# Optimization experiments

Measured on AMD Instinct MI355X. Metric: run time of the kernel, lower is better.

## Reference

```python
import jax, jax.numpy as jnp
import numpy as np

B, N, D, H = 8, 2048, 1024, 1024

def setup_inputs() -> dict:
    key = jax.random.key(0)
    ks = jax.random.split(key, 7)
    s = 1.0 / np.sqrt(D)
    return {
        "x": jax.random.normal(ks[0], (B, N, D), dtype=jnp.float32),
        "Wq": jax.random.uniform(ks[1], (D, H), jnp.float32, -s, s),
        "bq": jax.random.uniform(ks[2], (H,), jnp.float32, -s, s),
        "Wk": jax.random.uniform(ks[3], (D, H), jnp.float32, -s, s),
        "bk": jax.random.uniform(ks[4], (H,), jnp.float32, -s, s),
        "Wv": jax.random.uniform(ks[5], (D, H), jnp.float32, -s, s),
        "bv": jax.random.uniform(ks[6], (H,), jnp.float32, -s, s),
    }

def reference(x, Wq, bq, Wk, bk, Wv, bv):
    # q, k, v: [B, N, H]
    q = jnp.einsum('bnd,dh->bnh', x, Wq) + bq
    k = jnp.einsum('bnd,dh->bnh', x, Wk) + bk
    v = jnp.einsum('bnd,dh->bnh', x, Wv) + bv
    scale = 1.0 / jnp.sqrt(jnp.asarray(q.shape[-1], q.dtype))
    score = jnp.einsum('bqh,bkh->bqk', q, k) * scale  # [B, N, N]
    causal = jnp.tril(jnp.ones((q.shape[1], q.shape[1]), dtype=bool))
    score = jnp.where(causal, score, -jnp.inf)
    attn = jax.nn.softmax(score, axis=-1)
    # dropout p=0.0 -> identity (deterministic reference)
    return jnp.einsum('bqk,bkh->bqh', attn, v)
```

## Files before the change

kernel.cpp:

```cpp
#include <hip/hip_runtime.h>
#include <hip/hip_bf16.h>
#include <stdint.h>

#define BB 8
#define NN 2048
#define DD 1024
#define HH 1024

using f32x4 = __attribute__((ext_vector_type(4))) float;
using s16x8 = __attribute__((ext_vector_type(8))) short;

__device__ __forceinline__ short f2bf(float f){
  union { float f; uint32_t u; } v; v.f = f;
  uint32_t r = (v.u + 0x7fffu + ((v.u >> 16) & 1u)) >> 16;
  return (short)r;
}
__device__ __forceinline__ float bf2f(short s){
  union { uint32_t u; float f; } v; v.u = ((uint32_t)(uint16_t)s) << 16; return v.f;
}

#define MFMA(a,b,c) __builtin_amdgcn_mfma_f32_16x16x32_bf16((a),(b),(c),0,0,0)

#define GL16(gp, lp) __builtin_amdgcn_global_load_lds( \
    (const __attribute__((address_space(1))) void*)(gp), \
    (__attribute__((address_space(3))) void*)(lp), 16, 0, 0)

__global__ __launch_bounds__(256) void k_conv_x(const float* __restrict__ x,
                                                short* __restrict__ xb){
  int gid = blockIdx.x*256 + threadIdx.x;
  const float4* xv = (const float4*)x;
  float4 a = xv[(size_t)gid*2], b2 = xv[(size_t)gid*2+1];
  s16x8 o;
  o[0]=f2bf(a.x);  o[1]=f2bf(a.y);  o[2]=f2bf(a.z);  o[3]=f2bf(a.w);
  o[4]=f2bf(b2.x); o[5]=f2bf(b2.y); o[6]=f2bf(b2.z); o[7]=f2bf(b2.w);
  *(s16x8*)(xb + (size_t)gid*8) = o;
}

__global__ __launch_bounds__(256) void k_conv_w(const float* __restrict__ Wq,
                                                const float* __restrict__ Wk,
                                                const float* __restrict__ Wv,
                                                short* __restrict__ Wt){
  __shared__ float tile[64][65];
  int bx = blockIdx.x; int mat = bx >> 8; int ti = bx & 255;
  int d0 = (ti >> 4) << 6, h0 = (ti & 15) << 6;
  const float* W = (mat==0) ? Wq : (mat==1 ? Wk : Wv);
  int t = threadIdx.x;
  for (int i=0;i<16;i++){ int e = i*256 + t; int r = e>>6, c = e&63;
    tile[r][c] = W[(size_t)(d0+r)*HH + h0 + c]; }
  __syncthreads();
  for (int i=0;i<16;i++){ int e = i*256 + t; int r = e>>6, c = e&63;
    Wt[(size_t)(mat*HH + h0 + r)*DD + d0 + c] = f2bf(tile[c][r]); }
}

__global__ __launch_bounds__(512,2) void k_gemm(const short* __restrict__ Aw,
                                                const short* __restrict__ Bw,
                                                const float* __restrict__ bq,
                                                const float* __restrict__ bk,
                                                const float* __restrict__ bv,
                                                short* __restrict__ Qw,
                                                short* __restrict__ Kw,
                                                short* __restrict__ Vt){
  __shared__ short Al[4][256*32];
  __shared__ short Bl[4][256*32];
  const int t = threadIdx.x, l = t & 63, w = t >> 6;
  const int g = l >> 4, c = l & 15;
  const int bid = blockIdx.x;
  const int bm = (bid & 7)*8 + ((bid >> 3) & 7);
  const int bn = bid >> 6;
  const int m0 = bm << 8, c0 = bn << 8;
  const int wr = w >> 2, wc = w & 3;
  f32x4 acc[8][4] = {};

  const int sr = t >> 2, sch = t & 3;
  const int u0 = sch ^ ((sr >> 1) & 3);
  const int u1 = sch ^ (((sr + 128) >> 1) & 3);
  const short* A0 = Aw + (size_t)(m0 + sr)*DD + u0*8;
  const short* A1 = Aw + (size_t)(m0 + sr + 128)*DD + u1*8;
  const short* B0 = Bw + (size_t)(c0 + sr)*DD + u0*8;
  const short* B1 = Bw + (size_t)(c0 + sr + 128)*DD + u1*8;
  const int d0b = sr*64 + sch*16, d1b = (sr+128)*64 + sch*16;
  auto stage = [&](int kt){
    int s = kt & 3, ko = kt*32;
    GL16(A0 + ko, (char*)&Al[s][0] + d0b);
    GL16(A1 + ko, (char*)&Al[s][0] + d1b);
    GL16(B0 + ko, (char*)&Bl[s][0] + d0b);
    GL16(B1 + ko, (char*)&Bl[s][0] + d1b);
  };

  int aoff[8], boff[4];
  #pragma unroll
  for (int mi=0;mi<8;mi++){
    int row = wr*128 + mi*16 + c;
    aoff[mi] = row*32 + (g ^ ((row>>1)&3))*8;
  }
  #pragma unroll
  for (int ni=0;ni<4;ni++){
    int row = wc*64 + ni*16 + c;
    boff[ni] = row*32 + (g ^ ((row>>1)&3))*8;
  }

  auto body = [&](int kt, bool dostage){
    int s = kt & 3;
    __builtin_amdgcn_sched_barrier(0);
    __builtin_amdgcn_s_barrier();
    __builtin_amdgcn_sched_barrier(0);
    s16x8 bfr[4], af[8];
    #pragma unroll
    for (int ni=0;ni<4;ni++) bfr[ni] = *(const s16x8*)&Bl[s][boff[ni]];
    #pragma unroll
    for (int mi=0;mi<8;mi++) af[mi] = *(const s16x8*)&Al[s][aoff[mi]];
    if (dostage) stage(kt+3);
    __builtin_amdgcn_s_setprio(1);
    #pragma unroll
    for (int mi=0;mi<8;mi++)
      #pragma unroll
      for (int ni=0;ni<4;ni++)
        acc[mi][ni] = MFMA(bfr[ni], af[mi], acc[mi][ni]);
    __builtin_amdgcn_s_setprio(0);
  };

  stage(0); stage(1); stage(2);
  for (int kt = 0; kt < 30; ++kt){
    asm volatile("s_waitcnt vmcnt(8)" ::: "memory");
    body(kt, kt < 29);
  }
  asm volatile("s_waitcnt vmcnt(4)" ::: "memory");
  body(30, false);
  asm volatile("s_waitcnt vmcnt(0)" ::: "memory");
  body(31, false);

  const int mat = bn >> 2;
  const float* bias = (mat==0) ? bq : (mat==1 ? bk : bv);
  if (mat < 2){
    short* Outp = (mat==0) ? Qw : Kw;
    #pragma unroll
    for (int ni=0;ni<4;ni++){
      int col0 = (bn & 3)*256 + wc*64 + ni*16 + g*4;
      float4 bv4 = *(const float4*)&bias[col0];
      #pragma unroll
      for (int mi=0;mi<8;mi++){
        int orow = m0 + wr*128 + mi*16 + c;
        short4 pk;
        pk.x = f2bf(acc[mi][ni][0] + bv4.x);
        pk.y = f2bf(acc[mi][ni][1] + bv4.y);
        pk.z = f2bf(acc[mi][ni][2] + bv4.z);
        pk.w = f2bf(acc[mi][ni][3] + bv4.w);
        *(short4*)&Outp[(size_t)orow*HH + col0] = pk;
      }
    }
  } else {
    short* S = (w < 4) ? ((short*)&Al[0][0] + w*4352)
                       : ((short*)&Bl[0][0] + (w-4)*4352);
    const int bb = m0 >> 11;
    const int nbase = m0 & 2047;
    const int hglob0 = (bn & 3)*256 + wc*64;
    #pragma unroll
    for (int rr = 0; rr < 2; ++rr){
      const int R = 2*wr + rr;
      asm volatile("" ::: "memory");
      #pragma unroll
      for (int ni=0;ni<4;ni++){
        int col0 = hglob0 + ni*16 + g*4;
        float4 bv4 = *(const float4*)&bias[col0];
        #pragma unroll
        for (int mi2=0;mi2<4;mi2++){
          short4 pk;
          pk.x = f2bf(acc[rr*4+mi2][ni][0] + bv4.x);
          pk.y = f2bf(acc[rr*4+mi2][ni][1] + bv4.y);
          pk.z = f2bf(acc[rr*4+mi2][ni][2] + bv4.z);
          pk.w = f2bf(acc[rr*4+mi2][ni][3] + bv4.w);
          *(short4*)&S[(mi2*16 + c)*68 + ni*16 + g*4] = pk;
        }
      }
      asm volatile("" ::: "memory");
      #pragma unroll
      for (int k=0;k<8;++k){
        int hr = (l>>3) + k*8;
        int ng = l & 7;
        s16x8 sv;
        #pragma unroll
        for (int e=0;e<8;e++) sv[e] = S[(ng*8+e)*68 + hr];
        *(s16x8*)&Vt[((size_t)bb*HH + hglob0 + hr)*NN + nbase + R*64 + ng*8] = sv;
      }
    }
  }
}

__global__ __launch_bounds__(256) void k_s(const short* __restrict__ Qw,
                                           const short* __restrict__ Kw,
                                           short* __restrict__ Pp){
  __shared__ short Ql[128*32];
  __shared__ short Kl[128*32];
  const int t = threadIdx.x, l = t & 63, w = t >> 6;
  const int g = l >> 4, c = l & 15;
  int p = blockIdx.x; int b = p & 7; int ti = p >> 3;
  int tr = 0; while ((tr+1)*(tr+2)/2 <= ti) tr++;
  int tc = ti - tr*(tr+1)/2;
  const short* Aq = Qw + ((size_t)b*NN + tr*128)*HH;
  const short* Bk = Kw + ((size_t)b*NN + tc*128)*HH;
  const float SC_EXP = 0.04508422002783268f;
  const int wq = w >> 1, wk = w & 1;
  f32x4 acc[4][4] = {};

  const int srow0 = w*32 + (l >> 2), srow1 = srow0 + 16;
  const int su0 = (l & 3) ^ ((srow0 >> 1) & 3);
  const int su1 = (l & 3) ^ ((srow1 >> 1) & 3);
  const short* Qs0 = Aq + (size_t)srow0*HH + su0*8;
  const short* Qs1 = Aq + (size_t)srow1*HH + su1*8;
  const short* Ks0 = Bk + (size_t)srow0*HH + su0*8;
  const short* Ks1 = Bk + (size_t)srow1*HH + su1*8;
  const int rchunk = (g ^ ((c>>1)&3)) * 8;
  int qoff[4], koff[4];
  #pragma unroll
  for (int mi=0;mi<4;mi++) qoff[mi] = (wq*64 + mi*16 + c)*32 + rchunk;
  #pragma unroll
  for (int ni=0;ni<4;ni++) koff[ni] = (wk*64 + ni*16 + c)*32 + rchunk;

  for (int kt = 0; kt < 32; ++kt){
    int ko = kt*32;
    __syncthreads();
    GL16(Qs0 + ko, (char*)&Ql[(w*32)*32]);
    GL16(Qs1 + ko, (char*)&Ql[(w*32+16)*32]);
    GL16(Ks0 + ko, (char*)&Kl[(w*32)*32]);
    GL16(Ks1 + ko, (char*)&Kl[(w*32+16)*32]);
    __syncthreads();
    s16x8 qf[4], kf[4];
    #pragma unroll
    for (int mi=0;mi<4;mi++) qf[mi] = *(const s16x8*)&Ql[qoff[mi]];
    #pragma unroll
    for (int ni=0;ni<4;ni++) kf[ni] = *(const s16x8*)&Kl[koff[ni]];
    #pragma unroll
    for (int mi=0;mi<4;mi++)
      #pragma unroll
      for (int ni=0;ni<4;ni++)
        acc[mi][ni] = MFMA(kf[ni], qf[mi], acc[mi][ni]);
  }

  short* Pt = Pp + ((size_t)b*136 + ti)*16384;
  #pragma unroll
  for (int ni=0;ni<4;ni++){
    int pc0 = wk*64 + ni*16 + g*4;
    #pragma unroll
    for (int mi=0;mi<4;mi++){
      int pr = wq*64 + mi*16 + c;
      short4 pk;
      #pragma unroll
      for (int i=0;i<4;i++){
        bool keep = (tc*128 + pc0 + i) <= (tr*128 + pr);
        float pv = keep ? exp2f(acc[mi][ni][i]*SC_EXP) : 0.f;
        ((short*)&pk)[i] = f2bf(pv);
      }
      *(short4*)&Pt[pr*128 + pc0] = pk;
    }
  }
}

__global__ __launch_bounds__(256) void k_pv(const short* __restrict__ Pp,
                                            const short* __restrict__ Vt,
                                            float* __restrict__ out){
  __shared__ short Pl[128*32];
  __shared__ short Vl[128*32];
  const int t = threadIdx.x, l = t & 63, w = t >> 6;
  const int g = l >> 4, c = l & 15;
  int p = blockIdx.x;
  int r = p >> 8, j = p & 255;
  int tr, id;
  if      (r==0){ tr = j>>4;        id = (j&15); }
  else if (r==1){ tr = 15-(j>>4);   id = 16 + (j&15); }
  else if (r==2){ tr = (j&15);      id = 32 + (j>>4); }
  else          { tr = 15-(j&15);   id = 48 + (j>>4); }
  int b = id & 7, hc = id >> 3;
  const short* Pb = Pp + ((size_t)b*136 + tr*(tr+1)/2)*16384;
  const short* Bv = Vt + ((size_t)b*HH + hc*128)*NN;
  const int wp = w >> 1, wh = w & 1;
  f32x4 acc[4][4] = {};
  float ls[4] = {0.f,0.f,0.f,0.f};

  const int srow0 = w*32 + (l >> 2), srow1 = srow0 + 16;
  const int su0 = (l & 3) ^ ((srow0 >> 1) & 3);
  const int su1 = (l & 3) ^ ((srow1 >> 1) & 3);
  const int rchunk = (g ^ ((c>>1)&3)) * 8;
  int poff[4], voff[4];
  #pragma unroll
  for (int mi=0;mi<4;mi++) poff[mi] = (wp*64 + mi*16 + c)*32 + rchunk;
  #pragma unroll
  for (int ni=0;ni<4;ni++) voff[ni] = (wh*64 + ni*16 + c)*32 + rchunk;

  const int nst = (tr+1)*4;
  for (int kt = 0; kt < nst; ++kt){
    const short* Ps = Pb + (size_t)(kt>>2)*16384 + (kt&3)*32;
    __syncthreads();
    GL16(Ps + srow0*128 + su0*8, (char*)&Pl[(w*32)*32]);
    GL16(Ps + srow1*128 + su1*8, (char*)&Pl[(w*32+16)*32]);
    GL16(Bv + (size_t)srow0*NN + kt*32 + su0*8, (char*)&Vl[(w*32)*32]);
    GL16(Bv + (size_t)srow1*NN + kt*32 + su1*8, (char*)&Vl[(w*32+16)*32]);
    __syncthreads();
    s16x8 pf[4], vf[4];
    #pragma unroll
    for (int mi=0;mi<4;mi++) pf[mi] = *(const s16x8*)&Pl[poff[mi]];
    #pragma unroll
    for (int ni=0;ni<4;ni++) vf[ni] = *(const s16x8*)&Vl[voff[ni]];
    #pragma unroll
    for (int mi=0;mi<4;mi++)
      #pragma unroll
      for (int e=0;e<8;e++) ls[mi] += bf2f(pf[mi][e]);
    #pragma unroll
    for (int mi=0;mi<4;mi++)
      #pragma unroll
      for (int ni=0;ni<4;ni++)
        acc[mi][ni] = MFMA(vf[ni], pf[mi], acc[mi][ni]);
  }
  #pragma unroll
  for (int mi=0;mi<4;mi++){
    ls[mi] += __shfl_xor(ls[mi], 16);
    ls[mi] += __shfl_xor(ls[mi], 32);
  }
  #pragma unroll
  for (int mi=0;mi<4;mi++){
    float linv = 1.0f / ls[mi];
    int orow = tr*128 + wp*64 + mi*16 + c;
    #pragma unroll
    for (int ni=0;ni<4;ni++){
      int h0 = hc*128 + wh*64 + ni*16 + g*4;
      float4 o4;
      o4.x = acc[mi][ni][0]*linv; o4.y = acc[mi][ni][1]*linv;
      o4.z = acc[mi][ni][2]*linv; o4.w = acc[mi][ni][3]*linv;
      *(float4*)&out[((size_t)(b*NN + orow))*HH + h0] = o4;
    }
  }
}

extern "C" void kernel_launch(void* const* d_in, const int* in_sizes, int n_in,
                              void* d_out, int out_size, void* d_ws, size_t ws_size,
                              hipStream_t stream) {
  const float* x  = (const float*)d_in[0];
  const float* Wq = (const float*)d_in[1];
  const float* bq = (const float*)d_in[2];
  const float* Wk = (const float*)d_in[3];
  const float* bk = (const float*)d_in[4];
  const float* Wv = (const float*)d_in[5];
  const float* bv = (const float*)d_in[6];
  char* ws = (char*)d_ws;
  short* xb = (short*)(ws);
  short* Pp = (short*)(ws);
  short* Wt = (short*)(ws + 35651584u);
  short* Qw = (short*)(ws + 41943040u);
  short* Kw = (short*)(ws + 75497472u);
  short* Vt = (short*)(ws + 109051904u);

  k_conv_x<<<8192, 256, 0, stream>>>(x, xb);
  k_conv_w<<<768, 256, 0, stream>>>(Wq, Wk, Wv, Wt);
  k_gemm<<<768, 512, 0, stream>>>(xb, Wt, bq, bk, bv, Qw, Kw, Vt);
  k_s<<<1088, 256, 0, stream>>>(Qw, Kw, Pp);
  k_pv<<<1024, 256, 0, stream>>>(Pp, Vt, (float*)d_out);
}
```

Before: 286.1 us.

## Load QK and PV MFMA operands directly from global with register double-buffering

Both the score kernel and the PV kernel drop their LDS staging and barriers. Each lane now loads its MFMA fragments straight from global memory into registers, with two register buffers so the next k-step's loads are issued before the current MFMAs run. This removes the __syncthreads pairs and LDS traffic per k-step. In exchange, operand reuse across waves moves from LDS to the L1/L2 caches, and register pressure goes up.

```diff
diff --git a/kernel.cpp b/kernel.cpp
--- a/kernel.cpp
+++ b/kernel.cpp
@@ -189,51 +189,50 @@
 __global__ __launch_bounds__(256) void k_s(const short* __restrict__ Qw,
                                            const short* __restrict__ Kw,
                                            short* __restrict__ Pp){
-  __shared__ short Ql[128*32];
-  __shared__ short Kl[128*32];
   const int t = threadIdx.x, l = t & 63, w = t >> 6;
   const int g = l >> 4, c = l & 15;
   int p = blockIdx.x; int b = p & 7; int ti = p >> 3;
   int tr = 0; while ((tr+1)*(tr+2)/2 <= ti) tr++;
   int tc = ti - tr*(tr+1)/2;
-  const short* Aq = Qw + ((size_t)b*NN + tr*128)*HH;
-  const short* Bk = Kw + ((size_t)b*NN + tc*128)*HH;
   const float SC_EXP = 0.04508422002783268f;
   const int wq = w >> 1, wk = w & 1;
   f32x4 acc[4][4] = {};
 
-  const int srow0 = w*32 + (l >> 2), srow1 = srow0 + 16;
-  const int su0 = (l & 3) ^ ((srow0 >> 1) & 3);
-  const int su1 = (l & 3) ^ ((srow1 >> 1) & 3);
-  const short* Qs0 = Aq + (size_t)srow0*HH + su0*8;
-  const short* Qs1 = Aq + (size_t)srow1*HH + su1*8;
-  const short* Ks0 = Bk + (size_t)srow0*HH + su0*8;
-  const short* Ks1 = Bk + (size_t)srow1*HH + su1*8;
-  const int rchunk = (g ^ ((c>>1)&3)) * 8;
-  int qoff[4], koff[4];
-  #pragma unroll
-  for (int mi=0;mi<4;mi++) qoff[mi] = (wq*64 + mi*16 + c)*32 + rchunk;
-  #pragma unroll
-  for (int ni=0;ni<4;ni++) koff[ni] = (wk*64 + ni*16 + c)*32 + rchunk;
-
-  for (int kt = 0; kt < 32; ++kt){
-    int ko = kt*32;
-    __syncthreads();
-    GL16(Qs0 + ko, (char*)&Ql[(w*32)*32]);
-    GL16(Qs1 + ko, (char*)&Ql[(w*32+16)*32]);
-    GL16(Ks0 + ko, (char*)&Kl[(w*32)*32]);
-    GL16(Ks1 + ko, (char*)&Kl[(w*32+16)*32]);
-    __syncthreads();
-    s16x8 qf[4], kf[4];
-    #pragma unroll
-    for (int mi=0;mi<4;mi++) qf[mi] = *(const s16x8*)&Ql[qoff[mi]];
-    #pragma unroll
-    for (int ni=0;ni<4;ni++) kf[ni] = *(const s16x8*)&Kl[koff[ni]];
+  const short* qp[4]; const short* kp[4];
+  #pragma unroll
+  for (int mi=0;mi<4;mi++)
+    qp[mi] = Qw + ((size_t)(b*NN + tr*128 + wq*64 + mi*16 + c))*HH + g*8;
+  #pragma unroll
+  for (int ni=0;ni<4;ni++)
+    kp[ni] = Kw + ((size_t)(b*NN + tc*128 + wk*64 + ni*16 + c))*HH + g*8;
+
+  s16x8 qA[4], kA[4], qB[4], kB[4];
+  #pragma unroll
+  for (int ni=0;ni<4;ni++) kA[ni] = *(const s16x8*)(kp[ni]);
+  #pragma unroll
+  for (int mi=0;mi<4;mi++) qA[mi] = *(const s16x8*)(qp[mi]);
+
+  for (int kt2 = 0; kt2 < 16; ++kt2){
+    const int o1 = kt2*64 + 32;
+    const int o2 = (kt2 < 15) ? kt2*64 + 64 : 0;
+    #pragma unroll
+    for (int ni=0;ni<4;ni++) kB[ni] = *(const s16x8*)(kp[ni] + o1);
+    #pragma unroll
+    for (int mi=0;mi<4;mi++) qB[mi] = *(const s16x8*)(qp[mi] + o1);
     #pragma unroll
     for (int mi=0;mi<4;mi++)
       #pragma unroll
       for (int ni=0;ni<4;ni++)
-        acc[mi][ni] = MFMA(kf[ni], qf[mi], acc[mi][ni]);
+        acc[mi][ni] = MFMA(kA[ni], qA[mi], acc[mi][ni]);
+    #pragma unroll
+    for (int ni=0;ni<4;ni++) kA[ni] = *(const s16x8*)(kp[ni] + o2);
+    #pragma unroll
+    for (int mi=0;mi<4;mi++) qA[mi] = *(const s16x8*)(qp[mi] + o2);
+    #pragma unroll
+    for (int mi=0;mi<4;mi++)
+      #pragma unroll
+      for (int ni=0;ni<4;ni++)
+        acc[mi][ni] = MFMA(kB[ni], qB[mi], acc[mi][ni]);
   }
 
   short* Pt = Pp + ((size_t)b*136 + ti)*16384;
@@ -258,8 +257,6 @@
 __global__ __launch_bounds__(256) void k_pv(const short* __restrict__ Pp,
                                             const short* __restrict__ Vt,
                                             float* __restrict__ out){
-  __shared__ short Pl[128*32];
-  __shared__ short Vl[128*32];
   const int t = threadIdx.x, l = t & 63, w = t >> 6;
   const int g = l >> 4, c = l & 15;
   int p = blockIdx.x;
@@ -271,45 +268,60 @@
   else          { tr = 15-(j&15);   id = 48 + (j>>4); }
   int b = id & 7, hc = id >> 3;
   const short* Pb = Pp + ((size_t)b*136 + tr*(tr+1)/2)*16384;
-  const short* Bv = Vt + ((size_t)b*HH + hc*128)*NN;
   const int wp = w >> 1, wh = w & 1;
   f32x4 acc[4][4] = {};
   float ls[4] = {0.f,0.f,0.f,0.f};
 
-  const int srow0 = w*32 + (l >> 2), srow1 = srow0 + 16;
-  const int su0 = (l & 3) ^ ((srow0 >> 1) & 3);
-  const int su1 = (l & 3) ^ ((srow1 >> 1) & 3);
-  const int rchunk = (g ^ ((c>>1)&3)) * 8;
-  int poff[4], voff[4];
-  #pragma unroll
-  for (int mi=0;mi<4;mi++) poff[mi] = (wp*64 + mi*16 + c)*32 + rchunk;
-  #pragma unroll
-  for (int ni=0;ni<4;ni++) voff[ni] = (wh*64 + ni*16 + c)*32 + rchunk;
+  int prow[4];
+  #pragma unroll
+  for (int mi=0;mi<4;mi++) prow[mi] = (wp*64 + mi*16 + c)*128 + g*8;
+  const short* vp[4];
+  #pragma unroll
+  for (int ni=0;ni<4;ni++)
+    vp[ni] = Vt + ((size_t)(b*HH + hc*128 + wh*64 + ni*16 + c))*NN + g*8;
 
   const int nst = (tr+1)*4;
-  for (int kt = 0; kt < nst; ++kt){
-    const short* Ps = Pb + (size_t)(kt>>2)*16384 + (kt&3)*32;
-    __syncthreads();
-    GL16(Ps + srow0*128 + su0*8, (char*)&Pl[(w*32)*32]);
-    GL16(Ps + srow1*128 + su1*8, (char*)&Pl[(w*32+16)*32]);
-    GL16(Bv + (size_t)srow0*NN + kt*32 + su0*8, (char*)&Vl[(w*32)*32]);
-    GL16(Bv + (size_t)srow1*NN + kt*32 + su1*8, (char*)&Vl[(w*32+16)*32]);
-    __syncthreads();
-    s16x8 pf[4], vf[4];
-    #pragma unroll
-    for (int mi=0;mi<4;mi++) pf[mi] = *(const s16x8*)&Pl[poff[mi]];
-    #pragma unroll
-    for (int ni=0;ni<4;ni++) vf[ni] = *(const s16x8*)&Vl[voff[ni]];
+  s16x8 pA[4], vA[4], pB[4], vB[4];
+  #pragma unroll
+  for (int mi=0;mi<4;mi++) pA[mi] = *(const s16x8*)(Pb + prow[mi]);
+  #pragma unroll
+  for (int ni=0;ni<4;ni++) vA[ni] = *(const s16x8*)(vp[ni]);
+
+  for (int kt = 0; kt < nst; kt += 2){
+    const int k1 = kt + 1;
+    const short* P1 = Pb + (size_t)(k1>>2)*16384 + (k1&3)*32;
+    #pragma unroll
+    for (int mi=0;mi<4;mi++) pB[mi] = *(const s16x8*)(P1 + prow[mi]);
+    #pragma unroll
+    for (int ni=0;ni<4;ni++) vB[ni] = *(const s16x8*)(vp[ni] + k1*32);
+    #pragma unroll
+    for (int mi=0;mi<4;mi++){
+      #pragma unroll
+      for (int e=0;e<8;e++) ls[mi] += bf2f(pA[mi][e]);
+    }
     #pragma unroll
     for (int mi=0;mi<4;mi++)
       #pragma unroll
-      for (int e=0;e<8;e++) ls[mi] += bf2f(pf[mi][e]);
+      for (int ni=0;ni<4;ni++)
+        acc[mi][ni] = MFMA(vA[ni], pA[mi], acc[mi][ni]);
+    const int k2 = (kt + 2 < nst) ? kt + 2 : 0;
+    const short* P2 = Pb + (size_t)(k2>>2)*16384 + (k2&3)*32;
+    #pragma unroll
+    for (int mi=0;mi<4;mi++) pA[mi] = *(const s16x8*)(P2 + prow[mi]);
+    #pragma unroll
+    for (int ni=0;ni<4;ni++) vA[ni] = *(const s16x8*)(vp[ni] + k2*32);
+    #pragma unroll
+    for (int mi=0;mi<4;mi++){
+      #pragma unroll
+      for (int e=0;e<8;e++) ls[mi] += bf2f(pB[mi][e]);
+    }
     #pragma unroll
     for (int mi=0;mi<4;mi++)
       #pragma unroll
       for (int ni=0;ni<4;ni++)
-        acc[mi][ni] = MFMA(vf[ni], pf[mi], acc[mi][ni]);
-  }
+        acc[mi][ni] = MFMA(vB[ni], pB[mi], acc[mi][ni]);
+  }
+
   #pragma unroll
   for (int mi=0;mi<4;mi++){
     ls[mi] += __shfl_xor(ls[mi], 16);
```

After: 477.9 us. +67.1%, slower.

## Widen score and PV tiles to 128x256 with 512-thread blocks

Applied to the files above, without the earlier changes.

Both the score kernel and the P·V kernel now use 128x256 tiles computed by 8 waves instead of 128x128 tiles with 4 waves. The causal tiling groups key tiles in pairs of 128, which cuts the number of tiles and reloads of Q and P per output. The P buffer layout changes to 256-wide strips and the workspace offset of Wt is moved to fit. The trade-off is more wasted work on masked diagonal pairs and fewer blocks, which may hurt load balance.

```diff
diff --git a/kernel.cpp b/kernel.cpp
--- a/kernel.cpp
+++ b/kernel.cpp
@@ -186,29 +186,27 @@
   }
 }
 
-__global__ __launch_bounds__(256) void k_s(const short* __restrict__ Qw,
+__global__ __launch_bounds__(512) void k_s(const short* __restrict__ Qw,
                                            const short* __restrict__ Kw,
                                            short* __restrict__ Pp){
   __shared__ short Ql[128*32];
-  __shared__ short Kl[128*32];
+  __shared__ short Kl[256*32];
   const int t = threadIdx.x, l = t & 63, w = t >> 6;
   const int g = l >> 4, c = l & 15;
-  int p = blockIdx.x; int b = p & 7; int ti = p >> 3;
-  int tr = 0; while ((tr+1)*(tr+2)/2 <= ti) tr++;
-  int tc = ti - tr*(tr+1)/2;
-  const short* Aq = Qw + ((size_t)b*NN + tr*128)*HH;
-  const short* Bk = Kw + ((size_t)b*NN + tc*128)*HH;
+  int p = blockIdx.x; int b = p & 7; int si = p >> 3;
+  int tr = 0; while ((((tr+2)*(tr+2)) >> 2) <= si) tr++;
+  int tcp = si - (((tr+1)*(tr+1)) >> 2);
   const float SC_EXP = 0.04508422002783268f;
-  const int wq = w >> 1, wk = w & 1;
+  const int wq = w >> 2, wk = w & 3;
   f32x4 acc[4][4] = {};
 
-  const int srow0 = w*32 + (l >> 2), srow1 = srow0 + 16;
-  const int su0 = (l & 3) ^ ((srow0 >> 1) & 3);
-  const int su1 = (l & 3) ^ ((srow1 >> 1) & 3);
-  const short* Qs0 = Aq + (size_t)srow0*HH + su0*8;
-  const short* Qs1 = Aq + (size_t)srow1*HH + su1*8;
-  const short* Ks0 = Bk + (size_t)srow0*HH + su0*8;
-  const short* Ks1 = Bk + (size_t)srow1*HH + su1*8;
+  const int sr = t >> 2, sch = t & 3;
+  const int su  = sch ^ ((sr >> 1) & 3);
+  const int su2 = sch ^ (((sr + 128) >> 1) & 3);
+  const short* Qs  = Qw + ((size_t)(b*NN + tr*128  + sr))*HH + su*8;
+  const short* Ks0 = Kw + ((size_t)(b*NN + tcp*256 + sr))*HH + su*8;
+  const short* Ks1 = Kw + ((size_t)(b*NN + tcp*256 + sr + 128))*HH + su2*8;
+
   const int rchunk = (g ^ ((c>>1)&3)) * 8;
   int qoff[4], koff[4];
   #pragma unroll
@@ -219,16 +217,15 @@
   for (int kt = 0; kt < 32; ++kt){
     int ko = kt*32;
     __syncthreads();
-    GL16(Qs0 + ko, (char*)&Ql[(w*32)*32]);
-    GL16(Qs1 + ko, (char*)&Ql[(w*32+16)*32]);
-    GL16(Ks0 + ko, (char*)&Kl[(w*32)*32]);
-    GL16(Ks1 + ko, (char*)&Kl[(w*32+16)*32]);
+    GL16(Qs  + ko, (char*)Ql + t*16);
+    GL16(Ks0 + ko, (char*)Kl + t*16);
+    GL16(Ks1 + ko, (char*)Kl + 8192 + t*16);
     __syncthreads();
     s16x8 qf[4], kf[4];
     #pragma unroll
+    for (int ni=0;ni<4;ni++) kf[ni] = *(const s16x8*)&Kl[koff[ni]];
+    #pragma unroll
     for (int mi=0;mi<4;mi++) qf[mi] = *(const s16x8*)&Ql[qoff[mi]];
-    #pragma unroll
-    for (int ni=0;ni<4;ni++) kf[ni] = *(const s16x8*)&Kl[koff[ni]];
     #pragma unroll
     for (int mi=0;mi<4;mi++)
       #pragma unroll
@@ -236,7 +233,7 @@
         acc[mi][ni] = MFMA(kf[ni], qf[mi], acc[mi][ni]);
   }
 
-  short* Pt = Pp + ((size_t)b*136 + ti)*16384;
+  short* Pt = Pp + ((size_t)(b*72 + si))*32768;
   #pragma unroll
   for (int ni=0;ni<4;ni++){
     int pc0 = wk*64 + ni*16 + g*4;
@@ -246,64 +243,63 @@
       short4 pk;
       #pragma unroll
       for (int i=0;i<4;i++){
-        bool keep = (tc*128 + pc0 + i) <= (tr*128 + pr);
+        bool keep = (tcp*256 + pc0 + i) <= (tr*128 + pr);
         float pv = keep ? exp2f(acc[mi][ni][i]*SC_EXP) : 0.f;
         ((short*)&pk)[i] = f2bf(pv);
       }
-      *(short4*)&Pt[pr*128 + pc0] = pk;
-    }
-  }
-}
-
-__global__ __launch_bounds__(256) void k_pv(const short* __restrict__ Pp,
+      *(short4*)&Pt[pr*256 + pc0] = pk;
+    }
+  }
+}
+
+__global__ __launch_bounds__(512) void k_pv(const short* __restrict__ Pp,
                                             const short* __restrict__ Vt,
                                             float* __restrict__ out){
   __shared__ short Pl[128*32];
-  __shared__ short Vl[128*32];
+  __shared__ short Vl[256*32];
   const int t = threadIdx.x, l = t & 63, w = t >> 6;
   const int g = l >> 4, c = l & 15;
   int p = blockIdx.x;
   int r = p >> 8, j = p & 255;
-  int tr, id;
-  if      (r==0){ tr = j>>4;        id = (j&15); }
-  else if (r==1){ tr = 15-(j>>4);   id = 16 + (j&15); }
-  else if (r==2){ tr = (j&15);      id = 32 + (j>>4); }
-  else          { tr = 15-(j&15);   id = 48 + (j>>4); }
+  int tr = r ? (15 - (j >> 4)) : (j >> 4);
+  int id = r ? (16 + (j & 15)) : (j & 15);
   int b = id & 7, hc = id >> 3;
-  const short* Pb = Pp + ((size_t)b*136 + tr*(tr+1)/2)*16384;
-  const short* Bv = Vt + ((size_t)b*HH + hc*128)*NN;
-  const int wp = w >> 1, wh = w & 1;
+  const short* Pb = Pp + ((size_t)(b*72 + (((tr+1)*(tr+1))>>2)))*32768;
+  const int wq = w >> 2, wh = w & 3;
   f32x4 acc[4][4] = {};
   float ls[4] = {0.f,0.f,0.f,0.f};
 
-  const int srow0 = w*32 + (l >> 2), srow1 = srow0 + 16;
-  const int su0 = (l & 3) ^ ((srow0 >> 1) & 3);
-  const int su1 = (l & 3) ^ ((srow1 >> 1) & 3);
+  const int sr = t >> 2, sch = t & 3;
+  const int su  = sch ^ ((sr >> 1) & 3);
+  const int su2 = sch ^ (((sr + 128) >> 1) & 3);
+  const short* Vs0 = Vt + ((size_t)(b*HH + hc*256 + sr))*NN + su*8;
+  const short* Vs1 = Vt + ((size_t)(b*HH + hc*256 + sr + 128))*NN + su2*8;
+
   const int rchunk = (g ^ ((c>>1)&3)) * 8;
   int poff[4], voff[4];
   #pragma unroll
-  for (int mi=0;mi<4;mi++) poff[mi] = (wp*64 + mi*16 + c)*32 + rchunk;
+  for (int mi=0;mi<4;mi++) poff[mi] = (wq*64 + mi*16 + c)*32 + rchunk;
   #pragma unroll
   for (int ni=0;ni<4;ni++) voff[ni] = (wh*64 + ni*16 + c)*32 + rchunk;
 
-  const int nst = (tr+1)*4;
+  const int nst = ((tr + 2) >> 1) * 8;
   for (int kt = 0; kt < nst; ++kt){
-    const short* Ps = Pb + (size_t)(kt>>2)*16384 + (kt&3)*32;
+    const short* Ps = Pb + (size_t)(kt>>3)*32768 + (kt&7)*32;
     __syncthreads();
-    GL16(Ps + srow0*128 + su0*8, (char*)&Pl[(w*32)*32]);
-    GL16(Ps + srow1*128 + su1*8, (char*)&Pl[(w*32+16)*32]);
-    GL16(Bv + (size_t)srow0*NN + kt*32 + su0*8, (char*)&Vl[(w*32)*32]);
-    GL16(Bv + (size_t)srow1*NN + kt*32 + su1*8, (char*)&Vl[(w*32+16)*32]);
+    GL16(Ps + sr*256 + su*8, (char*)Pl + t*16);
+    GL16(Vs0 + kt*32, (char*)Vl + t*16);
+    GL16(Vs1 + kt*32, (char*)Vl + 8192 + t*16);
     __syncthreads();
     s16x8 pf[4], vf[4];
     #pragma unroll
+    for (int ni=0;ni<4;ni++) vf[ni] = *(const s16x8*)&Vl[voff[ni]];
+    #pragma unroll
     for (int mi=0;mi<4;mi++) pf[mi] = *(const s16x8*)&Pl[poff[mi]];
     #pragma unroll
-    for (int ni=0;ni<4;ni++) vf[ni] = *(const s16x8*)&Vl[voff[ni]];
-    #pragma unroll
-    for (int mi=0;mi<4;mi++)
+    for (int mi=0;mi<4;mi++){
       #pragma unroll
       for (int e=0;e<8;e++) ls[mi] += bf2f(pf[mi][e]);
+    }
     #pragma unroll
     for (int mi=0;mi<4;mi++)
       #pragma unroll
@@ -318,10 +314,10 @@
   #pragma unroll
   for (int mi=0;mi<4;mi++){
     float linv = 1.0f / ls[mi];
-    int orow = tr*128 + wp*64 + mi*16 + c;
+    int orow = tr*128 + wq*64 + mi*16 + c;
     #pragma unroll
     for (int ni=0;ni<4;ni++){
-      int h0 = hc*128 + wh*64 + ni*16 + g*4;
+      int h0 = hc*256 + wh*64 + ni*16 + g*4;
       float4 o4;
       o4.x = acc[mi][ni][0]*linv; o4.y = acc[mi][ni][1]*linv;
       o4.z = acc[mi][ni][2]*linv; o4.w = acc[mi][ni][3]*linv;
@@ -343,7 +339,7 @@
   char* ws = (char*)d_ws;
   short* xb = (short*)(ws);
   short* Pp = (short*)(ws);
-  short* Wt = (short*)(ws + 35651584u);
+  short* Wt = (short*)(ws + 33554432u);
   short* Qw = (short*)(ws + 41943040u);
   short* Kw = (short*)(ws + 75497472u);
   short* Vt = (short*)(ws + 109051904u);
@@ -351,6 +347,6 @@
   k_conv_x<<<8192, 256, 0, stream>>>(x, xb);
   k_conv_w<<<768, 256, 0, stream>>>(Wq, Wk, Wv, Wt);
   k_gemm<<<768, 512, 0, stream>>>(xb, Wt, bq, bk, bv, Qw, Kw, Vt);
-  k_s<<<1088, 256, 0, stream>>>(Qw, Kw, Pp);
-  k_pv<<<1024, 256, 0, stream>>>(Pp, Vt, (float*)d_out);
-}
+  k_s<<<576, 512, 0, stream>>>(Qw, Kw, Pp);
+  k_pv<<<512, 512, 0, stream>>>(Pp, Vt, (float*)d_out);
+}
```

Result: no change. 281.4 us, median of 2 (-1.6%).
